# Kernel optimization log

Hardware: AMD Instinct MI355X
Metric: run time of the kernel (lower is better)

The kernel has to match this reference:

```python
import jax, jax.numpy as jnp
import numpy as np

N_TX, N_CARD, N_MERCH = 200000, 50000, 10000
E = 200000
TX_IN, EMB, H = 128, 64, 128
N_LAYERS, N_ETYPES = 2, 4  # etypes: 0 card->tx, 1 tx->card, 2 merch->tx, 3 tx->merch


def setup_inputs() -> dict:
    key = jax.random.key(0)
    ks = jax.random.split(key, 24)
    s = 0.05
    inp = {
        "tx_x": jax.random.normal(ks[0], (N_TX, TX_IN), jnp.float32),
        "card_ids": jnp.arange(N_CARD, dtype=jnp.int64),
        "merch_ids": jnp.arange(N_MERCH, dtype=jnp.int64),
        "e_card": jax.random.randint(ks[1], (E,), 0, N_CARD),
        "e_tx_c": jnp.arange(E, dtype=jnp.int64),
        "e_merch": jax.random.randint(ks[2], (E,), 0, N_MERCH),
        "e_tx_m": jnp.arange(E, dtype=jnp.int64),
        # parameters
        "card_emb": jax.random.normal(ks[3], (N_CARD, EMB), jnp.float32) * s,
        "merch_emb": jax.random.normal(ks[4], (N_MERCH, EMB), jnp.float32) * s,
        "card_proj_W": jax.random.normal(ks[5], (EMB, H), jnp.float32) * s,
        "card_proj_b": jnp.zeros((H,), jnp.float32),
        "merch_proj_W": jax.random.normal(ks[6], (EMB, H), jnp.float32) * s,
        "merch_proj_b": jnp.zeros((H,), jnp.float32),
        "tx_W": jax.random.normal(ks[7], (TX_IN, H), jnp.float32) * s,
        "tx_b": jnp.zeros((H,), jnp.float32),
        "conv_Wl": jax.random.normal(ks[8], (N_LAYERS, N_ETYPES, H, H), jnp.float32) * s,
        "conv_bl": jnp.zeros((N_LAYERS, N_ETYPES, H), jnp.float32),
        "conv_Wr": jax.random.normal(ks[9], (N_LAYERS, N_ETYPES, H, H), jnp.float32) * s,
        "h1_W": jax.random.normal(ks[10], (H, H), jnp.float32) * s,
        "h1_b": jnp.zeros((H,), jnp.float32),
        "h2_W": jax.random.normal(ks[11], (H, 1), jnp.float32) * s,
        "h2_b": jnp.zeros((1,), jnp.float32),
    }
    return inp


def _sage(x_src, x_dst, src, dst, Wl, bl, Wr, n_dst):
    # PyG SAGEConv: mean-aggregate neighbor features, then lin_l(agg)+lin_r(x_dst)
    agg = jax.ops.segment_sum(x_src[src], dst, num_segments=n_dst)
    cnt = jax.ops.segment_sum(jnp.ones((src.shape[0],), x_src.dtype), dst, num_segments=n_dst)
    mean = agg / jnp.maximum(cnt, 1.0)[:, None]
    return mean @ Wl + bl + x_dst @ Wr


def reference(tx_x, card_ids, merch_ids, e_card, e_tx_c, e_merch, e_tx_m,
              card_emb, merch_emb, card_proj_W, card_proj_b, merch_proj_W, merch_proj_b,
              tx_W, tx_b, conv_Wl, conv_bl, conv_Wr, h1_W, h1_b, h2_W, h2_b):
    # input encoders (dropout inactive at eval)
    h_tx = jax.nn.relu(tx_x @ tx_W + tx_b)
    h_card = card_emb[card_ids] @ card_proj_W + card_proj_b
    h_merch = merch_emb[merch_ids] @ merch_proj_W + merch_proj_b

    for l in range(N_LAYERS):
        Wl, bl, Wr = conv_Wl[l], conv_bl[l], conv_Wr[l]
        # HeteroConv aggr='sum' across edge types sharing a dst type
        o_tx = (_sage(h_card, h_tx, e_card, e_tx_c, Wl[0], bl[0], Wr[0], N_TX)
                + _sage(h_merch, h_tx, e_merch, e_tx_m, Wl[2], bl[2], Wr[2], N_TX))
        o_card = _sage(h_tx, h_card, e_tx_c, e_card, Wl[1], bl[1], Wr[1], N_CARD)
        o_merch = _sage(h_tx, h_merch, e_tx_m, e_merch, Wl[3], bl[3], Wr[3], N_MERCH)
        h_tx, h_card, h_merch = jax.nn.relu(o_tx), jax.nn.relu(o_card), jax.nn.relu(o_merch)

    logits = (jax.nn.relu(h_tx @ h1_W + h1_b) @ h2_W + h2_b).reshape(-1)
    return logits
```

## Files before the change

kernel.cpp:

```cpp
#include <hip/hip_runtime.h>


#define N_TX    200000
#define N_CARD  50000
#define N_MERCH 10000
#define NE      200000

typedef __attribute__((ext_vector_type(8))) short short8;
typedef __attribute__((ext_vector_type(4))) float f32x4;

__device__ inline unsigned short f2b(float f) {
    unsigned u = __builtin_bit_cast(unsigned, f);
    unsigned r = (u + 0x7fffu + ((u >> 16) & 1u)) >> 16;
    return (unsigned short)r;
}
__device__ inline float b2f(unsigned short s) {
    return __builtin_bit_cast(float, (unsigned)s << 16);
}

__global__ __launch_bounds__(256, 2) void mfma_gemm(
    const void* __restrict__ A1, int a1_f32, const int* __restrict__ rowIdx1,
    int K1, const unsigned short* __restrict__ WT1,
    const void* __restrict__ A2, int K2, const unsigned short* __restrict__ WT2,
    const float* __restrict__ bias,
    const unsigned short* __restrict__ P1, const int* __restrict__ I1,
    const unsigned short* __restrict__ P2, const int* __restrict__ I2,
    int do_relu, const float* __restrict__ h2W, const float* __restrict__ h2b,
    void* __restrict__ OUT, int M)
{
    __shared__ unsigned short WTs[128 * 136];
    const int tid  = threadIdx.x;
    const int wave = tid >> 6;
    const int lane = tid & 63;
    const int quad = lane >> 4;
    const int l15  = lane & 15;
    const int base = blockIdx.x * 128;

    f32x4 acc[2][8];
#pragma unroll
    for (int mt = 0; mt < 2; ++mt)
#pragma unroll
        for (int nt = 0; nt < 8; ++nt)
            acc[mt][nt] = (f32x4){0.f, 0.f, 0.f, 0.f};

    for (int pass = 0; pass < 2; ++pass) {
        const void* A = (pass == 0) ? A1 : A2;
        if (!A) break;
        const int K = (pass == 0) ? K1 : K2;
        const unsigned short* WTg = (pass == 0) ? WT1 : WT2;
        const int* rIdx = (pass == 0) ? rowIdx1 : nullptr;
        const int a_f32 = (pass == 0) ? a1_f32 : 0;
        const int stride = K + 8;
        const int nkk = K >> 5;
        const int ksh = (K == 128) ? 7 : 6;

        __syncthreads();
        for (int i = tid * 8; i < (K << 7); i += 2048) {
            int row = i >> ksh;
            int off = i & (K - 1);
            *reinterpret_cast<short8*>(&WTs[row * stride + off]) =
                *reinterpret_cast<const short8*>(WTg + i);
        }
        __syncthreads();

        short8 af[2][4];
#pragma unroll
        for (int mt = 0; mt < 2; ++mt) {
            int r = base + wave * 32 + mt * 16 + l15;
            int rc = (r < M) ? r : 0;
            int ar = rIdx ? rIdx[rc] : rc;
            if (a_f32) {
                const float* ap = (const float*)A + (size_t)ar * K + quad * 8;
#pragma unroll
                for (int kk = 0; kk < 4; ++kk) if (kk < nkk) {
                    float4 u = *reinterpret_cast<const float4*>(ap + kk * 32);
                    float4 v = *reinterpret_cast<const float4*>(ap + kk * 32 + 4);
                    short8 t;
                    t[0] = (short)f2b(u.x); t[1] = (short)f2b(u.y);
                    t[2] = (short)f2b(u.z); t[3] = (short)f2b(u.w);
                    t[4] = (short)f2b(v.x); t[5] = (short)f2b(v.y);
                    t[6] = (short)f2b(v.z); t[7] = (short)f2b(v.w);
                    af[mt][kk] = t;
                }
            } else {
                const unsigned short* ap =
                    (const unsigned short*)A + (size_t)ar * K + quad * 8;
#pragma unroll
                for (int kk = 0; kk < 4; ++kk) if (kk < nkk)
                    af[mt][kk] = *reinterpret_cast<const short8*>(ap + kk * 32);
            }
        }

#pragma unroll
        for (int nt = 0; nt < 8; ++nt) {
            short8 bf[4];
            const unsigned short* bp = &WTs[(nt * 16 + l15) * stride + quad * 8];
#pragma unroll
            for (int kk = 0; kk < 4; ++kk) if (kk < nkk)
                bf[kk] = *reinterpret_cast<const short8*>(bp + kk * 32);
#pragma unroll
            for (int mt = 0; mt < 2; ++mt)
#pragma unroll
                for (int kk = 0; kk < 4; ++kk) if (kk < nkk)
                    acc[mt][nt] = __builtin_amdgcn_mfma_f32_16x16x32_bf16(
                        af[mt][kk], bf[kk], acc[mt][nt], 0, 0, 0);
        }
    }

    float bias_v[8], h2wv[8];
#pragma unroll
    for (int nt = 0; nt < 8; ++nt) {
        int col = nt * 16 + l15;
        bias_v[nt] = bias ? bias[col] : 0.f;
        h2wv[nt]   = h2W  ? h2W[col]  : 0.f;
    }
    unsigned short* OUTb = (unsigned short*)OUT;
    float* OUTf = (float*)OUT;
#pragma unroll
    for (int mt = 0; mt < 2; ++mt) {
        int rbase = base + wave * 32 + mt * 16 + quad * 4;
#pragma unroll
        for (int reg = 0; reg < 4; ++reg) {
            int r = rbase + reg;
            bool valid = r < M;
            int rc = valid ? r : 0;
            size_t i1 = P1 ? (size_t)I1[rc] * 128 : 0;
            size_t i2 = P2 ? (size_t)I2[rc] * 128 : 0;
            float hsum = 0.f;
#pragma unroll
            for (int nt = 0; nt < 8; ++nt) {
                int col = nt * 16 + l15;
                float o = acc[mt][nt][reg] + bias_v[nt];
                if (P1) o += b2f(P1[i1 + col]);
                if (P2) o += b2f(P2[i2 + col]);
                if (do_relu) o = fmaxf(o, 0.f);
                if (h2W) hsum += o * h2wv[nt];
                else if (valid) OUTb[(size_t)r * 128 + col] = f2b(o);
            }
            if (h2W) {
                hsum += __shfl_xor(hsum, 1);
                hsum += __shfl_xor(hsum, 2);
                hsum += __shfl_xor(hsum, 4);
                hsum += __shfl_xor(hsum, 8);
                if (l15 == 0 && valid) OUTf[r] = hsum + h2b[0];
            }
        }
    }
}

__global__ __launch_bounds__(256) void convert_weights(
    const float* __restrict__ tx_W, const float* __restrict__ card_proj_W,
    const float* __restrict__ merch_proj_W, const float* __restrict__ h1_W,
    const float* __restrict__ conv_Wl, const float* __restrict__ conv_Wr,
    const float* __restrict__ conv_bl,
    unsigned short* __restrict__ WT, float* __restrict__ bsum)
{
    int job = blockIdx.y;
    int K = 128;
    const float* src = nullptr;
    const float* src2 = nullptr;
    if (job == 0) src = tx_W;
    else if (job == 1) { src = card_proj_W; K = 64; }
    else if (job == 2) { src = merch_proj_W; K = 64; }
    else if (job == 3) src = h1_W;
    else {
        int l = (job - 4) / 7, e = (job - 4) % 7;
        const float* Wl = conv_Wl + (size_t)l * 4 * 16384;
        const float* Wr = conv_Wr + (size_t)l * 4 * 16384;
        switch (e) {
            case 0: src = Wl; break;
            case 1: src = Wl + 16384; break;
            case 2: src = Wl + 2 * 16384; break;
            case 3: src = Wl + 3 * 16384; break;
            case 4: src = Wr + 16384; break;
            case 5: src = Wr + 3 * 16384; break;
            default:
                src = Wr; src2 = Wr + 2 * 16384;
                if (blockIdx.x == 0 && threadIdx.x < 128) {
                    const float* bl = conv_bl + (size_t)l * 4 * 128;
                    bsum[l * 128 + threadIdx.x] =
                        bl[threadIdx.x] + bl[2 * 128 + threadIdx.x];
                }
                break;
        }
    }
    int e = blockIdx.x * 256 + threadIdx.x;
    if (e < (K << 7)) {
        int n = (K == 128) ? (e >> 7) : (e >> 6);
        int k = e & (K - 1);
        float v = src[(size_t)k * 128 + n];
        if (src2) v += src2[(size_t)k * 128 + n];
        WT[(size_t)job * 16384 + n * K + k] = f2b(v);
    }
}

__global__ __launch_bounds__(256) void hist_kernel(
    const int* __restrict__ e_card, const int* __restrict__ e_merch,
    int* __restrict__ hist_c, int* __restrict__ hist_m, int E)
{
    int i = blockIdx.x * 256 + threadIdx.x;
    if (i < E) {
        atomicAdd(&hist_c[e_card[i]], 1);
        atomicAdd(&hist_m[e_merch[i]], 1);
    }
}

__global__ __launch_bounds__(1024) void scan2_kernel(
    const int* __restrict__ hist_c, int* __restrict__ offs_c, int* __restrict__ cur_c, int nc,
    const int* __restrict__ hist_m, int* __restrict__ offs_m, int* __restrict__ cur_m, int nm)
{
    const int* hist = (blockIdx.x == 0) ? hist_c : hist_m;
    int* offs = (blockIdx.x == 0) ? offs_c : offs_m;
    int* cursor = (blockIdx.x == 0) ? cur_c : cur_m;
    int n = (blockIdx.x == 0) ? nc : nm;
    __shared__ int wsum[16];
    __shared__ int s_carry;
    const int tid = threadIdx.x, lane = tid & 63, wid = tid >> 6;
    if (tid == 0) s_carry = 0;
    __syncthreads();
    for (int base = 0; base < n; base += 1024) {
        int i = base + tid;
        int v = (i < n) ? hist[i] : 0;
        int x = v;
#pragma unroll
        for (int d = 1; d < 64; d <<= 1) {
            int t = __shfl_up(x, d);
            if (lane >= d) x += t;
        }
        if (lane == 63) wsum[wid] = x;
        __syncthreads();
        if (wid == 0) {
            int y = (lane < 16) ? wsum[lane] : 0;
#pragma unroll
            for (int d = 1; d < 16; d <<= 1) {
                int t = __shfl_up(y, d);
                if (lane >= d) y += t;
            }
            if (lane < 16) wsum[lane] = y;
        }
        __syncthreads();
        int wbase = (wid > 0) ? wsum[wid - 1] : 0;
        int excl = s_carry + wbase + x - v;
        if (i < n) { offs[i] = excl; cursor[i] = excl; }
        __syncthreads();
        if (tid == 0) s_carry += wsum[15];
        __syncthreads();
    }
    if (threadIdx.x == 0) offs[n] = s_carry;
}

__global__ __launch_bounds__(256) void place_kernel(
    const int* __restrict__ e_card, const int* __restrict__ e_tx_c,
    const int* __restrict__ e_merch, const int* __restrict__ e_tx_m,
    int* __restrict__ cur_c, int* __restrict__ eidx_c,
    int* __restrict__ cur_m, int* __restrict__ eidx_m, int E)
{
    int i = blockIdx.x * 256 + threadIdx.x;
    if (i < E) {
        int pc = atomicAdd(&cur_c[e_card[i]], 1);
        eidx_c[pc] = e_tx_c[i];
        int pm = atomicAdd(&cur_m[e_merch[i]], 1);
        eidx_m[pm] = e_tx_m[i];
    }
}

__global__ __launch_bounds__(256) void gather_mean(
    const unsigned short* __restrict__ h_src, const int* __restrict__ offs,
    const int* __restrict__ eidx, unsigned short* __restrict__ out_mean, int n_dst)
{
    const int lane = threadIdx.x & 63;
    const int d = blockIdx.x * 4 + (threadIdx.x >> 6);
    if (d >= n_dst) return;
    const int s = offs[d], e = offs[d + 1];
    float a0 = 0.f, a1 = 0.f;
    for (int p = s; p < e; ++p) {
        int tx = eidx[p];
        unsigned v = *reinterpret_cast<const unsigned*>(
            h_src + (size_t)tx * 128 + lane * 2);
        a0 += b2f((unsigned short)(v & 0xffff));
        a1 += b2f((unsigned short)(v >> 16));
    }
    const float inv = (e > s) ? 1.0f / (float)(e - s) : 0.f;
    unsigned o = ((unsigned)f2b(a1 * inv) << 16) | f2b(a0 * inv);
    *reinterpret_cast<unsigned*>(out_mean + (size_t)d * 128 + lane * 2) = o;
}

extern "C" void kernel_launch(void* const* d_in, const int* in_sizes, int n_in,
                              void* d_out, int out_size, void* d_ws, size_t ws_size,
                              hipStream_t stream)
{
    const float* tx_x        = (const float*)d_in[0];
    const int*   card_ids    = (const int*)d_in[1];
    const int*   merch_ids   = (const int*)d_in[2];
    const int*   e_card      = (const int*)d_in[3];
    const int*   e_tx_c      = (const int*)d_in[4];
    const int*   e_merch     = (const int*)d_in[5];
    const int*   e_tx_m      = (const int*)d_in[6];
    const float* card_emb    = (const float*)d_in[7];
    const float* merch_emb   = (const float*)d_in[8];
    const float* card_proj_W = (const float*)d_in[9];
    const float* card_proj_b = (const float*)d_in[10];
    const float* merch_proj_W= (const float*)d_in[11];
    const float* merch_proj_b= (const float*)d_in[12];
    const float* tx_W        = (const float*)d_in[13];
    const float* tx_b        = (const float*)d_in[14];
    const float* conv_Wl     = (const float*)d_in[15];
    const float* conv_bl     = (const float*)d_in[16];
    const float* conv_Wr     = (const float*)d_in[17];
    const float* h1_W        = (const float*)d_in[18];
    const float* h1_b        = (const float*)d_in[19];
    const float* h2_W        = (const float*)d_in[20];
    const float* h2_b        = (const float*)d_in[21];

    char* wsb = (char*)d_ws;
    auto alloc = [&](size_t bytes) {
        char* p = wsb; wsb += (bytes + 255) & ~(size_t)255; return p;
    };
    unsigned short* h_tx       = (unsigned short*)alloc((size_t)N_TX * 128 * 2);
    unsigned short* h_card     = (unsigned short*)alloc((size_t)N_CARD * 128 * 2);
    unsigned short* h_merch    = (unsigned short*)alloc((size_t)N_MERCH * 128 * 2);
    unsigned short* p_card     = (unsigned short*)alloc((size_t)N_CARD * 128 * 2);
    unsigned short* p_merch    = (unsigned short*)alloc((size_t)N_MERCH * 128 * 2);
    unsigned short* mean_card  = (unsigned short*)alloc((size_t)N_CARD * 128 * 2);
    unsigned short* mean_merch = (unsigned short*)alloc((size_t)N_MERCH * 128 * 2);
    unsigned short* WT         = (unsigned short*)alloc((size_t)18 * 16384 * 2);
    float* bsum = (float*)alloc(2 * 128 * 4);
    int* hist_c = (int*)alloc((size_t)(N_CARD + N_MERCH) * 4);
    int* hist_m = hist_c + N_CARD;
    int* offs_c = (int*)alloc((size_t)(N_CARD + 1) * 4);
    int* cur_c  = (int*)alloc((size_t)N_CARD * 4);
    int* eidx_c = (int*)alloc((size_t)NE * 4);
    int* offs_m = (int*)alloc((size_t)(N_MERCH + 1) * 4);
    int* cur_m  = (int*)alloc((size_t)N_MERCH * 4);
    int* eidx_m = (int*)alloc((size_t)NE * 4);

    auto WTj = [&](int job) { return WT + (size_t)job * 16384; };

    auto gemm = [&](const void* A1, int a1f32, const int* ri, int K1,
                    const unsigned short* W1, const void* A2, int K2,
                    const unsigned short* W2, const float* bias,
                    const unsigned short* P1, const int* I1,
                    const unsigned short* P2, const int* I2, int relu,
                    const float* h2w, const float* h2bb, void* out, int M) {
        mfma_gemm<<<dim3((M + 127) / 128), dim3(256), 0, stream>>>(
            A1, a1f32, ri, K1, W1, A2, K2, W2, bias, P1, I1, P2, I2, relu,
            h2w, h2bb, out, M);
    };

    convert_weights<<<dim3(64, 18), dim3(256), 0, stream>>>(
        tx_W, card_proj_W, merch_proj_W, h1_W, conv_Wl, conv_Wr, conv_bl,
        WT, bsum);
    hipMemsetAsync(hist_c, 0, (size_t)(N_CARD + N_MERCH) * 4, stream);
    hist_kernel<<<dim3((NE + 255) / 256), dim3(256), 0, stream>>>(
        e_card, e_merch, hist_c, hist_m, NE);
    scan2_kernel<<<dim3(2), dim3(1024), 0, stream>>>(
        hist_c, offs_c, cur_c, N_CARD, hist_m, offs_m, cur_m, N_MERCH);
    place_kernel<<<dim3((NE + 255) / 256), dim3(256), 0, stream>>>(
        e_card, e_tx_c, e_merch, e_tx_m, cur_c, eidx_c, cur_m, eidx_m, NE);

    gemm(tx_x, 1, nullptr, 128, WTj(0), nullptr, 0, nullptr, tx_b,
         nullptr, nullptr, nullptr, nullptr, 1, nullptr, nullptr, h_tx, N_TX);
    gemm(card_emb, 1, card_ids, 64, WTj(1), nullptr, 0, nullptr, card_proj_b,
         nullptr, nullptr, nullptr, nullptr, 0, nullptr, nullptr, h_card, N_CARD);
    gemm(merch_emb, 1, merch_ids, 64, WTj(2), nullptr, 0, nullptr, merch_proj_b,
         nullptr, nullptr, nullptr, nullptr, 0, nullptr, nullptr, h_merch, N_MERCH);

    for (int l = 0; l < 2; ++l) {
        const float* bl = conv_bl + (size_t)l * 4 * 128;
        int j = 4 + l * 7;

        gather_mean<<<dim3((N_CARD + 3) / 4), dim3(256), 0, stream>>>(
            h_tx, offs_c, eidx_c, mean_card, N_CARD);
        gather_mean<<<dim3((N_MERCH + 3) / 4), dim3(256), 0, stream>>>(
            h_tx, offs_m, eidx_m, mean_merch, N_MERCH);

        gemm(h_card, 0, nullptr, 128, WTj(j + 0), nullptr, 0, nullptr, nullptr,
             nullptr, nullptr, nullptr, nullptr, 0, nullptr, nullptr, p_card, N_CARD);
        gemm(h_merch, 0, nullptr, 128, WTj(j + 2), nullptr, 0, nullptr, nullptr,
             nullptr, nullptr, nullptr, nullptr, 0, nullptr, nullptr, p_merch, N_MERCH);

        gemm(mean_card, 0, nullptr, 128, WTj(j + 1), h_card, 128, WTj(j + 4),
             bl + 1 * 128, nullptr, nullptr, nullptr, nullptr, 1,
             nullptr, nullptr, h_card, N_CARD);
        gemm(mean_merch, 0, nullptr, 128, WTj(j + 3), h_merch, 128, WTj(j + 5),
             bl + 3 * 128, nullptr, nullptr, nullptr, nullptr, 1,
             nullptr, nullptr, h_merch, N_MERCH);

        gemm(h_tx, 0, nullptr, 128, WTj(j + 6), nullptr, 0, nullptr,
             bsum + l * 128, p_card, e_card, p_merch, e_merch, 1,
             nullptr, nullptr, h_tx, N_TX);
    }

    gemm(h_tx, 0, nullptr, 128, WTj(3), nullptr, 0, nullptr, h1_b,
         nullptr, nullptr, nullptr, nullptr, 1, h2_W, h2_b, d_out, N_TX);
}
```

Before: 815.3 us.

## Stage GEMM epilogue through LDS for vectorized stores; vectorize gather_mean loads

The GEMM epilogue now writes the MFMA accumulators to shared memory as bf16, then re-reads them row-wise so each thread handles 8 contiguous columns. This turns the bias, residual-gather and output accesses into 16-byte vector loads and stores instead of scattered 2-byte ones. gather_mean now has each wave process 4 edges in parallel with 16-byte loads per lane and combines the partial sums with cross-lane shuffles. In exchange the epilogue adds two block barriers, and accumulators are rounded to bf16 before bias and residual addition, which costs a little precision.

```diff
diff --git a/kernel.cpp b/kernel.cpp
--- a/kernel.cpp
+++ b/kernel.cpp
@@ -107,43 +107,65 @@
         }
     }
 
-    float bias_v[8], h2wv[8];
-#pragma unroll
-    for (int nt = 0; nt < 8; ++nt) {
-        int col = nt * 16 + l15;
-        bias_v[nt] = bias ? bias[col] : 0.f;
-        h2wv[nt]   = h2W  ? h2W[col]  : 0.f;
+    __syncthreads();
+#pragma unroll
+    for (int mt = 0; mt < 2; ++mt) {
+        int lrow0 = wave * 32 + mt * 16 + quad * 4;
+#pragma unroll
+        for (int nt = 0; nt < 8; ++nt) {
+            int col = nt * 16 + l15;
+#pragma unroll
+            for (int reg = 0; reg < 4; ++reg)
+                WTs[(lrow0 + reg) * 136 + col] = f2b(acc[mt][nt][reg]);
+        }
+    }
+    __syncthreads();
+
+    const int c0 = l15 * 8;
+    float bias8[8], h2w8[8];
+#pragma unroll
+    for (int j = 0; j < 8; ++j) {
+        bias8[j] = bias ? bias[c0 + j] : 0.f;
+        h2w8[j]  = h2W  ? h2W[c0 + j]  : 0.f;
     }
     unsigned short* OUTb = (unsigned short*)OUT;
     float* OUTf = (float*)OUT;
-#pragma unroll
-    for (int mt = 0; mt < 2; ++mt) {
-        int rbase = base + wave * 32 + mt * 16 + quad * 4;
-#pragma unroll
-        for (int reg = 0; reg < 4; ++reg) {
-            int r = rbase + reg;
-            bool valid = r < M;
-            int rc = valid ? r : 0;
-            size_t i1 = P1 ? (size_t)I1[rc] * 128 : 0;
-            size_t i2 = P2 ? (size_t)I2[rc] * 128 : 0;
-            float hsum = 0.f;
-#pragma unroll
-            for (int nt = 0; nt < 8; ++nt) {
-                int col = nt * 16 + l15;
-                float o = acc[mt][nt][reg] + bias_v[nt];
-                if (P1) o += b2f(P1[i1 + col]);
-                if (P2) o += b2f(P2[i2 + col]);
-                if (do_relu) o = fmaxf(o, 0.f);
-                if (h2W) hsum += o * h2wv[nt];
-                else if (valid) OUTb[(size_t)r * 128 + col] = f2b(o);
-            }
-            if (h2W) {
-                hsum += __shfl_xor(hsum, 1);
-                hsum += __shfl_xor(hsum, 2);
-                hsum += __shfl_xor(hsum, 4);
-                hsum += __shfl_xor(hsum, 8);
-                if (l15 == 0 && valid) OUTf[r] = hsum + h2b[0];
-            }
+    const int rgrp = tid >> 4;
+#pragma unroll 4
+    for (int p = 0; p < 8; ++p) {
+        const int rloc = p * 16 + rgrp;
+        const int r = base + rloc;
+        const bool valid = r < M;
+        const int rc = valid ? r : 0;
+        short8 av = *reinterpret_cast<const short8*>(&WTs[rloc * 136 + c0]);
+        short8 p1v{}, p2v{};
+        if (P1) {
+            size_t i1 = (size_t)I1[rc] * 128;
+            p1v = *reinterpret_cast<const short8*>(P1 + i1 + c0);
+        }
+        if (P2) {
+            size_t i2 = (size_t)I2[rc] * 128;
+            p2v = *reinterpret_cast<const short8*>(P2 + i2 + c0);
+        }
+        float hsum = 0.f;
+        short8 ov;
+#pragma unroll
+        for (int j = 0; j < 8; ++j) {
+            float o = b2f((unsigned short)av[j]) + bias8[j];
+            if (P1) o += b2f((unsigned short)p1v[j]);
+            if (P2) o += b2f((unsigned short)p2v[j]);
+            if (do_relu) o = fmaxf(o, 0.f);
+            if (h2W) hsum += o * h2w8[j];
+            else ov[j] = (short)f2b(o);
+        }
+        if (h2W) {
+            hsum += __shfl_xor(hsum, 1);
+            hsum += __shfl_xor(hsum, 2);
+            hsum += __shfl_xor(hsum, 4);
+            hsum += __shfl_xor(hsum, 8);
+            if (l15 == 0 && valid) OUTf[r] = hsum + h2b[0];
+        } else if (valid) {
+            *reinterpret_cast<short8*>(OUTb + (size_t)r * 128 + c0) = ov;
         }
     }
 }
@@ -269,20 +291,31 @@
     const int* __restrict__ eidx, unsigned short* __restrict__ out_mean, int n_dst)
 {
     const int lane = threadIdx.x & 63;
+    const int l15 = lane & 15;
+    const int quad = lane >> 4;
     const int d = blockIdx.x * 4 + (threadIdx.x >> 6);
     if (d >= n_dst) return;
     const int s = offs[d], e = offs[d + 1];
-    float a0 = 0.f, a1 = 0.f;
-    for (int p = s; p < e; ++p) {
+    float a[8] = {0.f, 0.f, 0.f, 0.f, 0.f, 0.f, 0.f, 0.f};
+    for (int p = s + quad; p < e; p += 4) {
         int tx = eidx[p];
-        unsigned v = *reinterpret_cast<const unsigned*>(
-            h_src + (size_t)tx * 128 + lane * 2);
-        a0 += b2f((unsigned short)(v & 0xffff));
-        a1 += b2f((unsigned short)(v >> 16));
-    }
-    const float inv = (e > s) ? 1.0f / (float)(e - s) : 0.f;
-    unsigned o = ((unsigned)f2b(a1 * inv) << 16) | f2b(a0 * inv);
-    *reinterpret_cast<unsigned*>(out_mean + (size_t)d * 128 + lane * 2) = o;
+        short8 v = *reinterpret_cast<const short8*>(
+            h_src + (size_t)tx * 128 + l15 * 8);
+#pragma unroll
+        for (int j = 0; j < 8; ++j) a[j] += b2f((unsigned short)v[j]);
+    }
+#pragma unroll
+    for (int j = 0; j < 8; ++j) {
+        a[j] += __shfl_xor(a[j], 16);
+        a[j] += __shfl_xor(a[j], 32);
+    }
+    if (quad == 0) {
+        const float inv = (e > s) ? 1.0f / (float)(e - s) : 0.f;
+        short8 o;
+#pragma unroll
+        for (int j = 0; j < 8; ++j) o[j] = (short)f2b(a[j] * inv);
+        *reinterpret_cast<short8*>(out_mean + (size_t)d * 128 + l15 * 8) = o;
+    }
 }
 
 extern "C" void kernel_launch(void* const* d_in, const int* in_sizes, int n_in,
```

Result: faster. 724.6 us (-11.1%).
